# Performance work log

Hardware: AMD Instinct MI355X
Metric: run time of the kernel (lower is better)

## Reference

```python
import jax, jax.numpy as jnp
import numpy as np

LN_EPS = 1e-5


def layer_norm(x, g, b):
    mu = jnp.mean(x, axis=-1, keepdims=True)
    var = jnp.var(x, axis=-1, keepdims=True)
    return (x - mu) / jnp.sqrt(var + LN_EPS) * g + b


def balanced_assignment(scores):
    # scores: [T, E]. Assign exactly C = T//E tokens to each expert,
    # greedily per expert by affinity (emulates libbase.balanced_assignment's
    # equal-split output structure deterministically).
    T, E = scores.shape
    C = T // E
    taken = jnp.zeros((T,), dtype=bool)
    parts = []
    for e in range(E):  # small fixed loop over experts
        s = jnp.where(taken, -jnp.inf, scores[:, e])
        _, idx = jax.lax.top_k(s, C)
        parts.append(idx)
        taken = taken.at[idx].set(True)
    return jnp.concatenate(parts)  # [T], chunks of C tokens per expert


def setup_inputs() -> dict:
    key = jax.random.key(0)
    ks = jax.random.split(key, 4)
    B, S, D, F, E = 4, 2048, 1024, 4096, 8
    return {
        "x": jax.random.normal(ks[0], (B, S, D), dtype=jnp.float32),
        "centroids": jax.random.normal(ks[1], (E, D), dtype=jnp.float32) * 0.1,
        "ln_g": jnp.ones((D,), dtype=jnp.float32),
        "ln_b": jnp.zeros((D,), dtype=jnp.float32),
        "w1": jax.random.normal(ks[2], (E, D, F), dtype=jnp.float32) * 0.02,
        "b1": jnp.zeros((E, F), dtype=jnp.float32),
        "w2": jax.random.normal(ks[3], (E, F, D), dtype=jnp.float32) * 0.02,
        "b2": jnp.zeros((E, D), dtype=jnp.float32),
    }


def reference(x, centroids, ln_g, ln_b, w1, b1, w2, b2):
    D = x.shape[-1]
    feat = x.reshape(-1, D)                      # [T, D]
    T = feat.shape[0]
    E = centroids.shape[0]
    C = T // E

    # affinity scores under no_grad in the original
    norm = layer_norm(feat, ln_g, ln_b)
    scores = jax.lax.stop_gradient(norm @ centroids.T)   # [T, E]

    sort_by_expert = balanced_assignment(scores)          # [T]

    routed = feat[sort_by_expert].reshape(E, C, D)        # dispatch gather

    # expert FFN sublayer: residual + W2(gelu(W1(ln(x))))
    h = layer_norm(routed, ln_g, ln_b)
    h = jax.nn.gelu(jnp.einsum('ecd,edf->ecf', h, w1) + b1[:, None, :])
    h = jnp.einsum('ecf,efd->ecd', h, w2) + b2[:, None, :]
    out = routed + h                                      # [E, C, D]

    # inverse_sort scatter: undo the dispatch permutation
    inv = jnp.zeros((T,), dtype=jnp.int32).at[sort_by_expert].set(
        jnp.arange(T, dtype=jnp.int32))
    return out.reshape(T, D)[inv].reshape(x.shape)
```

## Files before the change

kernel.cpp:

```cpp
#include <hip/hip_runtime.h>
#include <hip/hip_bf16.h>
#include <stdint.h>


#define T_TOK 8192
#define DM    1024
#define FF    4096
#define NE    8
#define CAP   1024

typedef __attribute__((ext_vector_type(8))) __bf16 bf16x8;
typedef __attribute__((ext_vector_type(4))) float  f32x4;

__device__ __forceinline__ unsigned short f2bf(float f) {
  unsigned u = __float_as_uint(f);
  u += 0x7FFFu + ((u >> 16) & 1u);
  return (unsigned short)(u >> 16);
}
__device__ __forceinline__ void gload_lds16(const void* g, void* l) {
  __builtin_amdgcn_global_load_lds(
      (const __attribute__((address_space(1))) unsigned int*)(uintptr_t)g,
      (__attribute__((address_space(3))) unsigned int*)l, 16, 0, 0);
}

__global__ __launch_bounds__(256) void ln_scores_k(
    const float* __restrict__ x, const float* __restrict__ g,
    const float* __restrict__ b, const float* __restrict__ cent,
    unsigned short* __restrict__ nrm, float* __restrict__ scores) {
  const int t = blockIdx.x, tid = threadIdx.x;
  const int lane = tid & 63, w = tid >> 6;
  float4 v = ((const float4*)(x + (size_t)t * DM))[tid];
  float f0 = v.x, f1 = v.y, f2 = v.z, f3 = v.w;
  float s = f0 + f1 + f2 + f3;
  float sq = f0 * f0 + f1 * f1 + f2 * f2 + f3 * f3;
#pragma unroll
  for (int o = 32; o > 0; o >>= 1) { s += __shfl_xor(s, o); sq += __shfl_xor(sq, o); }
  __shared__ float red[8];
  if (lane == 0) { red[w] = s; red[4 + w] = sq; }
  __syncthreads();
  float S = red[0] + red[1] + red[2] + red[3];
  float SQ = red[4] + red[5] + red[6] + red[7];
  float mu = S * (1.0f / DM);
  float var = SQ * (1.0f / DM) - mu * mu;
  float rstd = rsqrtf(var + 1e-5f);
  float4 gv = ((const float4*)g)[tid];
  float4 bv = ((const float4*)b)[tid];
  float n0 = (f0 - mu) * rstd * gv.x + bv.x;
  float n1 = (f1 - mu) * rstd * gv.y + bv.y;
  float n2 = (f2 - mu) * rstd * gv.z + bv.z;
  float n3 = (f3 - mu) * rstd * gv.w + bv.w;
  ushort4 o4;
  o4.x = f2bf(n0); o4.y = f2bf(n1); o4.z = f2bf(n2); o4.w = f2bf(n3);
  ((ushort4*)(nrm + (size_t)t * DM))[tid] = o4;
  __shared__ float sred[4];
  for (int e = 0; e < NE; ++e) {
    float4 cv = ((const float4*)(cent + e * DM))[tid];
    float p = n0 * cv.x + n1 * cv.y + n2 * cv.z + n3 * cv.w;
#pragma unroll
    for (int o = 32; o > 0; o >>= 1) p += __shfl_xor(p, o);
    if (lane == 0) sred[w] = p;
    __syncthreads();
    if (tid == 0) scores[(size_t)e * T_TOK + t] = sred[0] + sred[1] + sred[2] + sred[3];
    __syncthreads();
  }
}

__device__ __forceinline__ void pivot_scan(const unsigned* hist, unsigned* S) {
  const int l = threadIdx.x;
  unsigned v0 = hist[4 * l], v1 = hist[4 * l + 1];
  unsigned v2 = hist[4 * l + 2], v3 = hist[4 * l + 3];
  unsigned own = v0 + v1 + v2 + v3;
  unsigned s = own;
#pragma unroll
  for (int off = 1; off < 64; off <<= 1) {
    unsigned t = __shfl_down(s, off);
    if (l + off < 64) s += t;
  }
  unsigned i3 = (s - own) + v3;
  unsigned i2 = i3 + v2;
  unsigned i1 = i2 + v1;
  unsigned i0 = i1 + v0;
  unsigned need = S[0];
  if (i0 >= need && i0 - v0 < need) { S[1] = 4 * l + 0; S[0] = need - (i0 - v0); }
  if (i1 >= need && i1 - v1 < need) { S[1] = 4 * l + 1; S[0] = need - (i1 - v1); }
  if (i2 >= need && i2 - v2 < need) { S[1] = 4 * l + 2; S[0] = need - (i2 - v2); }
  if (i3 >= need && i3 - v3 < need) { S[1] = 4 * l + 3; S[0] = need - (i3 - v3); }
}
__device__ __forceinline__ void tie_select(const unsigned* bmap, unsigned* S,
                                           int* tokdst, unsigned char* taken) {
  const int l = threadIdx.x;
  unsigned wds[4] = {bmap[4 * l], bmap[4 * l + 1], bmap[4 * l + 2], bmap[4 * l + 3]};
  unsigned cnt = __popc(wds[0]) + __popc(wds[1]) + __popc(wds[2]) + __popc(wds[3]);
  unsigned p = cnt;
#pragma unroll
  for (int off = 1; off < 64; off <<= 1) {
    unsigned t = __shfl_up(p, off);
    if (l >= off) p += t;
  }
  unsigned base = p - cnt;
  const unsigned r = S[0];
#pragma unroll
  for (int c = 0; c < 4; ++c) {
    unsigned word = wds[c];
    while (word && base < r) {
      int b = __ffs(word) - 1; word &= word - 1;
      int i = (4 * l + c) * 32 + b;
      unsigned pp = atomicAdd(&S[2], 1u);
      tokdst[pp] = i; taken[i] = 1;
      ++base;
    }
    base += __popc(word);
  }
}

__device__ void assign_body(const float* __restrict__ scores,
                            int* __restrict__ tok, char* smem) {
  unsigned*       key   = (unsigned*)smem;
  unsigned short* candA = (unsigned short*)(smem + 32768);
  unsigned short* candB = (unsigned short*)(smem + 49152);
  unsigned char*  taken = (unsigned char*)(smem + 65536);
  unsigned*       hist  = (unsigned*)(smem + 73728);
  unsigned*       bmap  = (unsigned*)(smem + 74752);
  unsigned*       S     = (unsigned*)(smem + 75776);
  const int tid = threadIdx.x;
  for (int i = tid; i < T_TOK; i += 1024) taken[i] = 0;
  __syncthreads();
  for (int e = 0; e < NE; ++e) {
    const float* se = scores + (size_t)e * T_TOK;
    if (tid < 256) hist[tid] = 0;
    if (tid == 0) { S[0] = CAP; S[2] = 0; S[4] = 0; }
    __syncthreads();
#pragma unroll
    for (int j = 0; j < 8; ++j) {
      int i = j * 1024 + tid;
      unsigned k = 0;
      if (!taken[i]) {
        unsigned bb = __float_as_uint(se[i]);
        k = (bb & 0x80000000u) ? ~bb : (bb | 0x80000000u);
      }
      key[i] = k;
      atomicAdd(&hist[k >> 24], 1u);
    }
    __syncthreads();
    if (tid < 64) pivot_scan(hist, S);
    __syncthreads();
    {
      const unsigned pb = S[1];
#pragma unroll
      for (int j = 0; j < 8; ++j) {
        int i = j * 1024 + tid;
        unsigned by = key[i] >> 24;
        if (by > pb) {
          unsigned p = atomicAdd(&S[2], 1u);
          tok[e * CAP + p] = i; taken[i] = 1;
        } else if (by == pb) {
          unsigned q = atomicAdd(&S[4], 1u);
          candA[q] = (unsigned short)i;
        }
      }
    }
    __syncthreads();
    unsigned short* cur = candA;
    unsigned short* nxt = candB;
    for (int shift = 16; shift >= 0; shift -= 8) {
      const unsigned m = S[4];
      __syncthreads();
      if (tid < 256) hist[tid] = 0;
      if (tid == 0) S[4] = 0;
      __syncthreads();
      for (unsigned q = tid; q < m; q += 1024)
        atomicAdd(&hist[(key[cur[q]] >> shift) & 255u], 1u);
      __syncthreads();
      if (tid < 64) pivot_scan(hist, S);
      __syncthreads();
      const unsigned pb = S[1];
      for (unsigned q = tid; q < m; q += 1024) {
        unsigned i = cur[q];
        unsigned by = (key[i] >> shift) & 255u;
        if (by > pb) {
          unsigned p = atomicAdd(&S[2], 1u);
          tok[e * CAP + p] = (int)i; taken[i] = 1;
        } else if (by == pb) {
          unsigned t2 = atomicAdd(&S[4], 1u);
          nxt[t2] = (unsigned short)i;
        }
      }
      __syncthreads();
      unsigned short* tmp = cur; cur = nxt; nxt = tmp;
    }
    if (tid < 256) bmap[tid] = 0;
    __syncthreads();
    {
      const unsigned m = S[4];
      for (unsigned q = tid; q < m; q += 1024) {
        unsigned i = cur[q];
        atomicOr(&bmap[i >> 5], 1u << (i & 31));
      }
    }
    __syncthreads();
    if (tid < 64) tie_select(bmap, S, tok + e * CAP, taken);
    __syncthreads();
  }
}

__global__ __launch_bounds__(1024) void fat_assign_transpose(
    const float* __restrict__ scores, int* __restrict__ tok,
    const float* __restrict__ w1, const float* __restrict__ w2,
    unsigned short* __restrict__ w1T, unsigned short* __restrict__ w2T) {
  __shared__ __align__(16) char smem[77824];
  if (blockIdx.x == 0) { assign_body(scores, tok, smem); return; }
  const int tix = blockIdx.x - 1;
  const int which = tix >> 11;
  const int r = tix & 2047;
  const int e = r >> 8;
  const int rr = r & 255;
  int K, N, nt, kt;
  const float* s;
  unsigned short* d;
  if (which == 0) { K = DM; N = FF; nt = rr & 31; kt = rr >> 5; s = w1; d = w1T; }
  else            { K = FF; N = DM; nt = rr & 7;  kt = rr >> 3; s = w2; d = w2T; }
  s += (size_t)e * K * N;
  d += (size_t)e * N * K;
  const int q = threadIdx.x >> 8, t2 = threadIdx.x & 255;
  const int k0 = kt * 128 + (q >> 1) * 64;
  const int n0 = nt * 128 + (q & 1) * 64;
  float (*t)[65] = (float (*)[65])(smem + q * 16640);
  for (int p = t2; p < 1024; p += 256) {
    int rw = p >> 4, c4 = (p & 15) * 4;
    float4 v = *(const float4*)(s + (size_t)(k0 + rw) * N + n0 + c4);
    t[c4 + 0][rw] = v.x; t[c4 + 1][rw] = v.y;
    t[c4 + 2][rw] = v.z; t[c4 + 3][rw] = v.w;
  }
  __syncthreads();
  for (int p = t2; p < 512; p += 256) {
    int c = p >> 3, r8 = (p & 7) * 8;
    unsigned short tmp[8];
#pragma unroll
    for (int i = 0; i < 8; ++i) tmp[i] = f2bf(t[c][r8 + i]);
    *(uint4*)(d + (size_t)(n0 + c) * K + k0 + r8) = *(const uint4*)tmp;
  }
}

template <int EPI, bool GATHER, int K, int N, int BM, int BN, int TPB,
          int WM, int WN>
__global__ __launch_bounds__(TPB, 2) void gemm_ring(
    const unsigned short* __restrict__ A, const unsigned short* __restrict__ Bt,
    const float* __restrict__ bias, const int* __restrict__ tok,
    const float* __restrict__ xres, void* __restrict__ Cout) {
  constexpr int NT  = K / 32;
  constexpr int RM  = BM / WM, RN = BN / WN;
  constexpr int MR  = RM / 16, NR = RN / 16;
  constexpr int ALD = (BM * 32) / (8 * TPB);
  constexpr int BLD = (BN * 32) / (8 * TPB);
  constexpr int LD  = ALD + BLD;
  constexpr int SLOT = (BM + BN) * 32;
  __shared__ __align__(16) unsigned short lds[3 * SLOT];
  __shared__ int tokl[BM];

  const int flat = blockIdx.x + gridDim.x * (blockIdx.y + gridDim.y * blockIdx.z);
  const int nwg = gridDim.x * gridDim.y * gridDim.z;
  const int nf = (flat & 7) * (nwg >> 3) + (flat >> 3);
  const int bx = nf % gridDim.x;
  const int rem = nf / gridDim.x;
  const int e  = rem / gridDim.y;
  const int n0 = bx * BN, m0 = (rem % gridDim.y) * BM;

  const int tid = threadIdx.x, lane = tid & 63, w = tid >> 6;
  const int wr = w / WN, wc = w % WN;
  const int lr = lane & 15, lk = lane >> 4;

  for (int i = tid; i < BM; i += TPB) tokl[i] = tok[e * CAP + m0 + i];
  __syncthreads();

  const unsigned short* aptr[ALD];
  const unsigned short* bptr[BLD];
  const unsigned short* Be = Bt + (size_t)e * N * K + (size_t)n0 * K;
#pragma unroll
  for (int i = 0; i < ALD; ++i) {
    int c = i * TPB + tid, row = c >> 2, sp = c & 3;
    int s = sp ^ ((row >> 1) & 3);
    size_t grow = GATHER ? (size_t)tokl[row] : (size_t)(e * CAP + m0 + row);
    aptr[i] = A + grow * K + s * 8;
  }
#pragma unroll
  for (int i = 0; i < BLD; ++i) {
    int c = i * TPB + tid, row = c >> 2, sp = c & 3;
    int s = sp ^ ((row >> 1) & 3);
    bptr[i] = Be + (size_t)row * K + s * 8;
  }
  auto stage = [&](int tile, int slot) {
    unsigned short* base = lds + (size_t)slot * SLOT;
#pragma unroll
    for (int i = 0; i < ALD; ++i)
      gload_lds16(aptr[i] + tile * 32, base + (i * TPB + tid) * 8);
#pragma unroll
    for (int i = 0; i < BLD; ++i)
      gload_lds16(bptr[i] + tile * 32, base + BM * 32 + (i * TPB + tid) * 8);
  };

  const int swz = (lr >> 1) & 3;
  const int afo = (wr * RM + lr) * 32 + (lk ^ swz) * 8;
  const int bfo = BM * 32 + (wc * RN + lr) * 32 + (lk ^ swz) * 8;

  f32x4 acc[MR][NR] = {};

  stage(0, 0); stage(1, 1);
  asm volatile("s_waitcnt vmcnt(%0)" :: "i"(LD) : "memory");
  __builtin_amdgcn_s_barrier();

  int slot = 0;
#pragma unroll 1
  for (int t = 0; t < NT; ++t) {
    const unsigned short* base = lds + (size_t)slot * SLOT;
    bf16x8 af[MR], bfr[NR];
#pragma unroll
    for (int mi = 0; mi < MR; ++mi)
      af[mi] = *(const bf16x8*)(base + afo + mi * 512);
#pragma unroll
    for (int ni = 0; ni < NR; ++ni)
      bfr[ni] = *(const bf16x8*)(base + bfo + ni * 512);
    if (t + 2 < NT) {
      int dst = slot - 1;
      if (dst < 0) dst = 2;
      stage(t + 2, dst);
      asm volatile("s_waitcnt vmcnt(%0)" :: "i"(LD) : "memory");
    } else if (t + 2 == NT) {
      asm volatile("s_waitcnt vmcnt(0)" ::: "memory");
    }
    __builtin_amdgcn_s_barrier();
    asm volatile("s_waitcnt lgkmcnt(0)" ::: "memory");
    __builtin_amdgcn_sched_barrier(0);
    __builtin_amdgcn_s_setprio(1);
#pragma unroll
    for (int mi = 0; mi < MR; ++mi)
#pragma unroll
      for (int ni = 0; ni < NR; ++ni)
        acc[mi][ni] = __builtin_amdgcn_mfma_f32_16x16x32_bf16(
            af[mi], bfr[ni], acc[mi][ni], 0, 0, 0);
    __builtin_amdgcn_s_setprio(0);
    __builtin_amdgcn_s_barrier();
    slot = (slot == 2) ? 0 : slot + 1;
  }

  const int lg = lane >> 4;
#pragma unroll
  for (int ni = 0; ni < NR; ++ni) {
    const int n = n0 + wc * RN + ni * 16 + lr;
    const float bb = bias[e * N + n];
#pragma unroll
    for (int mi = 0; mi < MR; ++mi) {
#pragma unroll
      for (int r = 0; r < 4; ++r) {
        const int ml = wr * RM + mi * 16 + lg * 4 + r;
        float v = acc[mi][ni][r] + bb;
        if (EPI == 1) {
          float z = 1.5957691216f * v + 0.07135481283f * v * v * v;
          float gl = v / (1.0f + __expf(-z));
          ((unsigned short*)Cout)[(size_t)(e * CAP + m0 + ml) * N + n] = f2bf(gl);
        } else {
          const int token = tokl[ml];
          v += xres[(size_t)token * DM + n];
          ((float*)Cout)[(size_t)token * (size_t)N + n] = v;
        }
      }
    }
  }
}

extern "C" void kernel_launch(void* const* d_in, const int* in_sizes, int n_in,
                              void* d_out, int out_size, void* d_ws, size_t ws_size,
                              hipStream_t stream) {
  const float* x    = (const float*)d_in[0];
  const float* cent = (const float*)d_in[1];
  const float* ln_g = (const float*)d_in[2];
  const float* ln_b = (const float*)d_in[3];
  const float* w1   = (const float*)d_in[4];
  const float* b1   = (const float*)d_in[5];
  const float* w2   = (const float*)d_in[6];
  const float* b2   = (const float*)d_in[7];
  float* out = (float*)d_out;

  char* ws = (char*)d_ws;
  size_t off = 0;
  unsigned short* w1T = (unsigned short*)(ws + off); off += (size_t)NE * FF * DM * 2;
  unsigned short* w2T = (unsigned short*)(ws + off); off += (size_t)NE * DM * FF * 2;
  unsigned short* nrm = (unsigned short*)(ws + off); off += (size_t)T_TOK * DM * 2;
  unsigned short* h1  = (unsigned short*)(ws + off); off += (size_t)T_TOK * FF * 2;
  float* scores       = (float*)(ws + off);          off += (size_t)NE * T_TOK * 4;
  int* tok            = (int*)(ws + off);            off += (size_t)T_TOK * 4;

  ln_scores_k<<<dim3(T_TOK), 256, 0, stream>>>(x, ln_g, ln_b, cent, nrm, scores);
  fat_assign_transpose<<<dim3(1 + 4096), 1024, 0, stream>>>(
      scores, tok, w1, w2, w1T, w2T);
  gemm_ring<1, true, DM, FF, 256, 128, 512, 4, 2>
      <<<dim3(FF / 128, CAP / 256, NE), 512, 0, stream>>>(nrm, w1T, b1, tok, nullptr, h1);
  gemm_ring<2, false, FF, DM, 128, 128, 256, 2, 2>
      <<<dim3(DM / 128, CAP / 128, NE), 256, 0, stream>>>(h1, w2T, b2, tok, x, out);
}
```

Measured before the change: 330.4 us.

## Track free-token list across experts instead of taken flags in assignment

Replaces the per-token taken bitmap and cached key array with a compacted free-list of unassigned token indices, so each expert's radix select only scans tokens that are still free. Surviving tokens are compacted with a ballot/prefix-sum into a second list, and keys are recomputed from global scores instead of being stored in LDS. This reduces work in later experts but adds extra barriers per 1024-token chunk and repeated global score reads in the refinement passes.

```diff
diff --git a/kernel.cpp b/kernel.cpp
--- a/kernel.cpp
+++ b/kernel.cpp
@@ -16,6 +16,13 @@
   unsigned u = __float_as_uint(f);
   u += 0x7FFFu + ((u >> 16) & 1u);
   return (unsigned short)(u >> 16);
+}
+__device__ __forceinline__ float keyf(float s) {
+  return s;
+}
+__device__ __forceinline__ unsigned keyu(float s) {
+  unsigned bb = __float_as_uint(s);
+  return (bb & 0x80000000u) ? ~bb : (bb | 0x80000000u);
 }
 __device__ __forceinline__ void gload_lds16(const void* g, void* l) {
   __builtin_amdgcn_global_load_lds(
@@ -65,8 +72,8 @@
   }
 }
 
-__device__ __forceinline__ void pivot_scan(const unsigned* hist, unsigned* S) {
-  const int l = threadIdx.x;
+__device__ __forceinline__ void pivot_scan(const unsigned* hist, unsigned* S,
+                                           int l) {
   unsigned v0 = hist[4 * l], v1 = hist[4 * l + 1];
   unsigned v2 = hist[4 * l + 2], v3 = hist[4 * l + 3];
   unsigned own = v0 + v1 + v2 + v3;
@@ -87,8 +94,8 @@
   if (i3 >= need && i3 - v3 < need) { S[1] = 4 * l + 3; S[0] = need - (i3 - v3); }
 }
 __device__ __forceinline__ void tie_select(const unsigned* bmap, unsigned* S,
-                                           int* tokdst, unsigned char* taken) {
-  const int l = threadIdx.x;
+                                           int* tokdst, unsigned short* nfl,
+                                           int l) {
   unsigned wds[4] = {bmap[4 * l], bmap[4 * l + 1], bmap[4 * l + 2], bmap[4 * l + 3]};
   unsigned cnt = __popc(wds[0]) + __popc(wds[1]) + __popc(wds[2]) + __popc(wds[3]);
   unsigned p = cnt;
@@ -102,63 +109,67 @@
 #pragma unroll
   for (int c = 0; c < 4; ++c) {
     unsigned word = wds[c];
-    while (word && base < r) {
+    while (word) {
       int b = __ffs(word) - 1; word &= word - 1;
       int i = (4 * l + c) * 32 + b;
-      unsigned pp = atomicAdd(&S[2], 1u);
-      tokdst[pp] = i; taken[i] = 1;
+      if (base < r) { unsigned pp = atomicAdd(&S[2], 1u); tokdst[pp] = i; }
+      else          { unsigned pp = atomicAdd(&S[5], 1u); nfl[pp] = (unsigned short)i; }
       ++base;
     }
-    base += __popc(word);
   }
 }
 
 __device__ void assign_body(const float* __restrict__ scores,
                             int* __restrict__ tok, char* smem) {
-  unsigned*       key   = (unsigned*)smem;
+  unsigned short* flA   = (unsigned short*)smem;
+  unsigned short* flB   = (unsigned short*)(smem + 16384);
   unsigned short* candA = (unsigned short*)(smem + 32768);
   unsigned short* candB = (unsigned short*)(smem + 49152);
-  unsigned char*  taken = (unsigned char*)(smem + 65536);
-  unsigned*       hist  = (unsigned*)(smem + 73728);
-  unsigned*       bmap  = (unsigned*)(smem + 74752);
-  unsigned*       S     = (unsigned*)(smem + 75776);
-  const int tid = threadIdx.x;
-  for (int i = tid; i < T_TOK; i += 1024) taken[i] = 0;
+  unsigned*       hist  = (unsigned*)(smem + 65536);
+  unsigned*       bmap  = (unsigned*)(smem + 66560);
+  unsigned*       wcnt  = (unsigned*)(smem + 67584);
+  unsigned*       S     = (unsigned*)(smem + 67648);
+  const int tid = threadIdx.x, lane = tid & 63, wv = tid >> 6;
+  unsigned short* fl = flA;
+  unsigned short* nfl = flB;
+  for (int i = tid; i < T_TOK; i += 1024) fl[i] = (unsigned short)i;
+  unsigned fc = T_TOK;
   __syncthreads();
   for (int e = 0; e < NE; ++e) {
     const float* se = scores + (size_t)e * T_TOK;
     if (tid < 256) hist[tid] = 0;
-    if (tid == 0) { S[0] = CAP; S[2] = 0; S[4] = 0; }
-    __syncthreads();
-#pragma unroll
-    for (int j = 0; j < 8; ++j) {
-      int i = j * 1024 + tid;
-      unsigned k = 0;
-      if (!taken[i]) {
-        unsigned bb = __float_as_uint(se[i]);
-        k = (bb & 0x80000000u) ? ~bb : (bb | 0x80000000u);
+    if (tid == 0) { S[0] = CAP; S[2] = 0; S[4] = 0; S[5] = 0; }
+    __syncthreads();
+    for (unsigned q = tid; q < fc; q += 1024)
+      atomicAdd(&hist[keyu(se[fl[q]]) >> 24], 1u);
+    __syncthreads();
+    if (tid < 64) pivot_scan(hist, S, tid);
+    __syncthreads();
+    const unsigned pb0 = S[1];
+    unsigned nbase = 0;
+    const unsigned nch = (fc + 1023) >> 10;
+    for (unsigned ch = 0; ch < nch; ++ch) {
+      const unsigned q = ch * 1024 + tid;
+      int i = -1; unsigned by = 0;
+      if (q < fc) { i = fl[q]; by = keyu(se[i]) >> 24; }
+      const bool win = (i >= 0) && (by > pb0);
+      const bool eq  = (i >= 0) && (by == pb0);
+      const bool sur = (i >= 0) && (by < pb0);
+      if (win) { unsigned p = atomicAdd(&S[2], 1u); tok[e * CAP + p] = i; }
+      if (eq)  { unsigned p = atomicAdd(&S[4], 1u); candA[p] = (unsigned short)i; }
+      unsigned long long sb = __ballot(sur);
+      if (lane == 0) wcnt[wv] = (unsigned)__popcll(sb);
+      __syncthreads();
+      unsigned base = 0, tot = 0;
+      for (int j = 0; j < 16; ++j) { unsigned u = wcnt[j]; tot += u; if (j < wv) base += u; }
+      if (sur) {
+        unsigned off = (unsigned)__popcll(sb & ((1ull << lane) - 1ull));
+        nfl[nbase + base + off] = (unsigned short)i;
       }
-      key[i] = k;
-      atomicAdd(&hist[k >> 24], 1u);
-    }
-    __syncthreads();
-    if (tid < 64) pivot_scan(hist, S);
-    __syncthreads();
-    {
-      const unsigned pb = S[1];
-#pragma unroll
-      for (int j = 0; j < 8; ++j) {
-        int i = j * 1024 + tid;
-        unsigned by = key[i] >> 24;
-        if (by > pb) {
-          unsigned p = atomicAdd(&S[2], 1u);
-          tok[e * CAP + p] = i; taken[i] = 1;
-        } else if (by == pb) {
-          unsigned q = atomicAdd(&S[4], 1u);
-          candA[q] = (unsigned short)i;
-        }
-      }
-    }
+      nbase += tot;
+      __syncthreads();
+    }
+    if (tid == 0) S[5] = nbase;
     __syncthreads();
     unsigned short* cur = candA;
     unsigned short* nxt = candB;
@@ -169,20 +180,20 @@
       if (tid == 0) S[4] = 0;
       __syncthreads();
       for (unsigned q = tid; q < m; q += 1024)
-        atomicAdd(&hist[(key[cur[q]] >> shift) & 255u], 1u);
-      __syncthreads();
-      if (tid < 64) pivot_scan(hist, S);
+        atomicAdd(&hist[(keyu(se[cur[q]]) >> shift) & 255u], 1u);
+      __syncthreads();
+      if (tid < 64) pivot_scan(hist, S, tid);
       __syncthreads();
       const unsigned pb = S[1];
       for (unsigned q = tid; q < m; q += 1024) {
         unsigned i = cur[q];
-        unsigned by = (key[i] >> shift) & 255u;
+        unsigned by = (keyu(se[i]) >> shift) & 255u;
         if (by > pb) {
-          unsigned p = atomicAdd(&S[2], 1u);
-          tok[e * CAP + p] = (int)i; taken[i] = 1;
+          unsigned p = atomicAdd(&S[2], 1u); tok[e * CAP + p] = (int)i;
         } else if (by == pb) {
-          unsigned t2 = atomicAdd(&S[4], 1u);
-          nxt[t2] = (unsigned short)i;
+          unsigned p = atomicAdd(&S[4], 1u); nxt[p] = (unsigned short)i;
+        } else {
+          unsigned p = atomicAdd(&S[5], 1u); nfl[p] = (unsigned short)i;
         }
       }
       __syncthreads();
@@ -198,7 +209,10 @@
       }
     }
     __syncthreads();
-    if (tid < 64) tie_select(bmap, S, tok + e * CAP, taken);
+    if (tid < 64) tie_select(bmap, S, tok + e * CAP, nfl, tid);
+    __syncthreads();
+    fc = S[5];
+    unsigned short* tmp = fl; fl = nfl; nfl = tmp;
     __syncthreads();
   }
 }
```

Result: no change. 332.9 us (+0.8%).
